# Optimization experiments

Measured on AMD Instinct MI355X. Metric: run time of the kernel, lower is better.

The kernel has to match this reference:

```python
import jax, jax.numpy as jnp
import numpy as np

NEG_INF = jnp.float32(-1e30)


def setup_inputs() -> dict:
    key = jax.random.key(0)
    ks = jax.random.split(key, 7)
    B, Lx, Lm, d = 4, 256, 256, 256
    return {
        "x": jax.random.normal(ks[0], (B, Lx, d), dtype=jnp.float32),
        "memory": jax.random.normal(ks[1], (B, Lm, d), dtype=jnp.float32),
        "memory_mask": jax.random.randint(ks[2], (B, Lm), 0, 2, dtype=jnp.int32),
        "ws1_w": jax.random.normal(ks[3], (d, d), dtype=jnp.float32) * 0.05,
        "ws1_b": jax.random.normal(ks[4], (d,), dtype=jnp.float32) * 0.05,
        "ws2_w": jax.random.normal(ks[5], (d, d), dtype=jnp.float32) * 0.05,
        "wst_w": jax.random.normal(ks[6], (1, d), dtype=jnp.float32) * 0.05,
    }


def reference(x, memory, memory_mask, ws1_w, ws1_b, ws2_w, wst_w):
    # x: [B, Lx, d], memory: [B, Lm, d]; torch Linear: y = x @ W.T + b
    item1 = jnp.einsum('bxd,ed->bxe', x, ws1_w) + ws1_b          # [B, Lx, d]
    item2 = jnp.einsum('bmd,ed->bme', memory, ws2_w)             # [B, Lm, d]
    item = jnp.tanh(item1[:, :, None, :] + item2[:, None, :, :])  # [B, Lx, Lm, d]
    S = jnp.einsum('bxmd,d->bxm', item, wst_w[0])                # [B, Lx, Lm]
    # agg_2_h uses the UNMASKED scores, softmax over Lx after transpose
    agg_2_h = jnp.einsum('bmx,bxd->bmd', jax.nn.softmax(S.transpose(0, 2, 1), axis=-1), x)
    # mask applied to S before the main attention readout
    S = jnp.where(memory_mask[:, None, :] == 0, NEG_INF, S)      # [B, Lx, Lm]
    out = jnp.einsum('bxm,bmd->bxd', jax.nn.softmax(S, axis=-1), memory)
    return (out, S, agg_2_h)
```

## Files before the change

kernel.cpp:

```cpp
#include <hip/hip_runtime.h>

static constexpr int NB = 4;
static constexpr int L  = 256;
static constexpr int D  = 256;

__device__ __forceinline__ float fast_rcp(float x) {
#if __has_builtin(__builtin_amdgcn_rcpf)
    return __builtin_amdgcn_rcpf(x);
#else
    return 1.0f / x;
#endif
}

__device__ __forceinline__ float fast_exp(float x) {
#if __has_builtin(__builtin_amdgcn_exp2f)
    return __builtin_amdgcn_exp2f(x * 1.4426950408889634f);
#else
    return __expf(x);
#endif
}

__device__ __forceinline__ float exp_2x(float x) {
#if __has_builtin(__builtin_amdgcn_exp2f)
    return __builtin_amdgcn_exp2f(x * 2.8853900817779268f);
#else
    return __expf(2.0f * x);
#endif
}

__global__ __launch_bounds__(256) void linear_kernel(
    const float* __restrict__ x, const float* __restrict__ mem,
    const float* __restrict__ w1, const float* __restrict__ b1,
    const float* __restrict__ w2,
    float* __restrict__ E1R, float* __restrict__ E2R)
{
    const int bid = blockIdx.x;
    const int rb  = (bid >> 3) * 32;
    const int cb  = (bid & 7) * 32;
    const int which = rb >= 1024;
    const int rloc  = which ? rb - 1024 : rb;
    const float* src = which ? mem : x;
    const float* W   = which ? w2  : w1;
    float*      dstR = which ? E2R : E1R;

    constexpr int P4 = 65;
    __shared__ __align__(16) float4 xs4[32 * P4];
    __shared__ __align__(16) float4 ws4[32 * P4];

    const int t = threadIdx.x;
    const float4* src4 = reinterpret_cast<const float4*>(src) + rloc * 64;
    const float4* Wg4  = reinterpret_cast<const float4*>(W)   + cb   * 64;
#pragma unroll
    for (int k = 0; k < 8; ++k) {
        int idx = k * 256 + t;
        int r = idx >> 6, c = idx & 63;
        xs4[r * P4 + c] = src4[r * 64 + c];
        ws4[r * P4 + c] = Wg4[r * 64 + c];
    }
    __syncthreads();

    const int rr = t >> 4, cc = t & 15;
    const float4* a0p = xs4 + rr * P4;
    const float4* a1p = xs4 + (rr + 16) * P4;
    const float4* w0p = ws4 + cc * P4;
    const float4* w1p = ws4 + (cc + 16) * P4;
    float acc00 = 0.f, acc01 = 0.f, acc10 = 0.f, acc11 = 0.f;
#pragma unroll 4
    for (int d4 = 0; d4 < 64; ++d4) {
        float4 a0 = a0p[d4], a1 = a1p[d4];
        float4 w0 = w0p[d4], w1 = w1p[d4];
        acc00 = fmaf(a0.x, w0.x, acc00); acc00 = fmaf(a0.y, w0.y, acc00);
        acc00 = fmaf(a0.z, w0.z, acc00); acc00 = fmaf(a0.w, w0.w, acc00);
        acc01 = fmaf(a0.x, w1.x, acc01); acc01 = fmaf(a0.y, w1.y, acc01);
        acc01 = fmaf(a0.z, w1.z, acc01); acc01 = fmaf(a0.w, w1.w, acc01);
        acc10 = fmaf(a1.x, w0.x, acc10); acc10 = fmaf(a1.y, w0.y, acc10);
        acc10 = fmaf(a1.z, w0.z, acc10); acc10 = fmaf(a1.w, w0.w, acc10);
        acc11 = fmaf(a1.x, w1.x, acc11); acc11 = fmaf(a1.y, w1.y, acc11);
        acc11 = fmaf(a1.z, w1.z, acc11); acc11 = fmaf(a1.w, w1.w, acc11);
    }
    const float bias0 = which ? 0.f : b1[cb + cc];
    const float bias1 = which ? 0.f : b1[cb + cc + 16];
    const int c0 = cb + cc, c1 = cb + cc + 16;
    const int rA = rloc + rr, rB = rloc + rr + 16;
    dstR[rA * D + c0] = exp_2x(acc00 + bias0);
    dstR[rA * D + c1] = exp_2x(acc01 + bias1);
    dstR[rB * D + c0] = exp_2x(acc10 + bias0);
    dstR[rB * D + c1] = exp_2x(acc11 + bias1);
}

__global__ __launch_bounds__(256) void score_kernel(
    const float* __restrict__ E1R, const float* __restrict__ E2R,
    const float* __restrict__ wst, const int* __restrict__ mask,
    float* __restrict__ Smask, float* __restrict__ ST)
{
    const int bid = blockIdx.x;
    const int p   = bid & 7, q = bid >> 3;
    const int b   = p >> 1;
    const int xg  = (q & 7) | ((p & 1) << 3);
    const int mg  = q >> 3;
    const int xt  = xg * 16, mt = mg * 32;
    const int base = b * L;
    const int t   = threadIdx.x;

    constexpr int P4 = 65;
    __shared__ __align__(16) float4 s1[16 * P4];
    __shared__ __align__(16) float4 s2[32 * P4];
    __shared__ float stile[32 * 17];

    const float4* e14 = reinterpret_cast<const float4*>(E1R) + (base + xt) * 64;
    const float4* e24 = reinterpret_cast<const float4*>(E2R) + (base + mt) * 64;
#pragma unroll
    for (int k = 0; k < 4; ++k) {
        int idx = k * 256 + t;
        int r = idx >> 6, c = idx & 63;
        s1[r * P4 + c] = e14[r * 64 + c];
    }
#pragma unroll
    for (int k = 0; k < 8; ++k) {
        int idx = k * 256 + t;
        int r = idx >> 6, c = idx & 63;
        s2[r * P4 + c] = e24[r * 64 + c];
    }
    __syncthreads();

    const float4* w4 = reinterpret_cast<const float4*>(wst);
    float W_tot;
    {
        float4 wv = w4[t & 63];
        float s = (wv.x + wv.y) + (wv.z + wv.w);
#pragma unroll
        for (int o = 32; o; o >>= 1) s += __shfl_xor(s, o);
        W_tot = s;
    }

    const int rr = t >> 4, cc = t & 15;
    const float4* ap  = s1 + rr * P4;
    const float4* b0p = s2 + cc * P4;
    const float4* b1p = s2 + (cc + 16) * P4;
    float acc0 = 0.f, acc1 = 0.f;
#pragma unroll 4
    for (int d4 = 0; d4 < 64; ++d4) {
        float4 a  = ap[d4];
        float4 b0 = b0p[d4], b1 = b1p[d4];
        float4 wv = w4[d4];
        acc0 = fmaf(wv.x, fast_rcp(fmaf(a.x, b0.x, 1.f)), acc0);
        acc0 = fmaf(wv.y, fast_rcp(fmaf(a.y, b0.y, 1.f)), acc0);
        acc0 = fmaf(wv.z, fast_rcp(fmaf(a.z, b0.z, 1.f)), acc0);
        acc0 = fmaf(wv.w, fast_rcp(fmaf(a.w, b0.w, 1.f)), acc0);
        acc1 = fmaf(wv.x, fast_rcp(fmaf(a.x, b1.x, 1.f)), acc1);
        acc1 = fmaf(wv.y, fast_rcp(fmaf(a.y, b1.y, 1.f)), acc1);
        acc1 = fmaf(wv.z, fast_rcp(fmaf(a.z, b1.z, 1.f)), acc1);
        acc1 = fmaf(wv.w, fast_rcp(fmaf(a.w, b1.w, 1.f)), acc1);
    }
    const float S0 = fmaf(-2.f, acc0, W_tot);
    const float S1 = fmaf(-2.f, acc1, W_tot);

    const int m0 = mt + cc, m1 = mt + cc + 16, x0 = xt + rr;
    Smask[((base + x0) << 8) + m0] = (mask[base + m0] == 0) ? -1e30f : S0;
    Smask[((base + x0) << 8) + m1] = (mask[base + m1] == 0) ? -1e30f : S1;

    stile[cc        * 17 + rr] = S0;
    stile[(cc + 16) * 17 + rr] = S1;
    __syncthreads();
#pragma unroll
    for (int k = 0; k < 2; ++k) {
        int idx = k * 256 + t;
        int mr = idx >> 4, xc = idx & 15;
        ST[((base + mt + mr) << 8) + xt + xc] = stile[mr * 17 + xc];
    }
}

__global__ __launch_bounds__(256) void attn_kernel(
    const float* __restrict__ x, const float* __restrict__ mem,
    const float* __restrict__ Smask, const float* __restrict__ ST,
    float* __restrict__ out, float* __restrict__ agg)
{
    const int bid  = blockIdx.x;
    const int p    = bid & 7, g = bid >> 3;
    const int side = p & 1,  b = p >> 1;
    const float* S = side ? ST : Smask;
    const float* V = side ? x  : mem;
    float*       o = side ? agg : out;
    const int base = b * L;
    const int row0 = g * 8;
    const int t = threadIdx.x, w = t >> 6, l = t & 63;

    __shared__ __align__(16) float  ps[8][L];
    __shared__ __align__(16) float4 part[8][4][64];

    float rs0, rs1;
#pragma unroll
    for (int rr = w, it = 0; rr < 8; rr += 4, ++it) {
        float4 sv = reinterpret_cast<const float4*>(S)[((base + row0 + rr) << 6) + l];
        float e0 = fast_exp(sv.x), e1 = fast_exp(sv.y);
        float e2 = fast_exp(sv.z), e3 = fast_exp(sv.w);
        reinterpret_cast<float4*>(ps[rr])[l] = make_float4(e0, e1, e2, e3);
        float s = (e0 + e1) + (e2 + e3);
#pragma unroll
        for (int off = 32; off; off >>= 1) s += __shfl_xor(s, off);
        if (it == 0) rs0 = fast_rcp(s); else rs1 = fast_rcp(s);
    }
    __syncthreads();

    const float4* V4 = reinterpret_cast<const float4*>(V) + base * 64;
    float4 acc[8];
#pragma unroll
    for (int r = 0; r < 8; ++r) acc[r] = make_float4(0.f, 0.f, 0.f, 0.f);

#pragma unroll 2
    for (int k4 = 0; k4 < 16; ++k4) {
        const int m0 = w * 64 + k4 * 4;
        float4 v0 = V4[(m0 + 0) * 64 + l];
        float4 v1 = V4[(m0 + 1) * 64 + l];
        float4 v2 = V4[(m0 + 2) * 64 + l];
        float4 v3 = V4[(m0 + 3) * 64 + l];
#pragma unroll
        for (int r = 0; r < 8; ++r) {
            float4 pr = *reinterpret_cast<const float4*>(&ps[r][m0]);
            acc[r].x = fmaf(pr.x, v0.x, acc[r].x); acc[r].y = fmaf(pr.x, v0.y, acc[r].y);
            acc[r].z = fmaf(pr.x, v0.z, acc[r].z); acc[r].w = fmaf(pr.x, v0.w, acc[r].w);
            acc[r].x = fmaf(pr.y, v1.x, acc[r].x); acc[r].y = fmaf(pr.y, v1.y, acc[r].y);
            acc[r].z = fmaf(pr.y, v1.z, acc[r].z); acc[r].w = fmaf(pr.y, v1.w, acc[r].w);
            acc[r].x = fmaf(pr.z, v2.x, acc[r].x); acc[r].y = fmaf(pr.z, v2.y, acc[r].y);
            acc[r].z = fmaf(pr.z, v2.z, acc[r].z); acc[r].w = fmaf(pr.z, v2.w, acc[r].w);
            acc[r].x = fmaf(pr.w, v3.x, acc[r].x); acc[r].y = fmaf(pr.w, v3.y, acc[r].y);
            acc[r].z = fmaf(pr.w, v3.z, acc[r].z); acc[r].w = fmaf(pr.w, v3.w, acc[r].w);
        }
    }
#pragma unroll
    for (int r = 0; r < 8; ++r) part[r][w][l] = acc[r];
    __syncthreads();

#pragma unroll
    for (int rr = w, it = 0; rr < 8; rr += 4, ++it) {
        float rs = (it == 0) ? rs0 : rs1;
        float4 q0 = part[rr][0][l], q1 = part[rr][1][l];
        float4 q2 = part[rr][2][l], q3 = part[rr][3][l];
        float4 ov;
        ov.x = ((q0.x + q1.x) + (q2.x + q3.x)) * rs;
        ov.y = ((q0.y + q1.y) + (q2.y + q3.y)) * rs;
        ov.z = ((q0.z + q1.z) + (q2.z + q3.z)) * rs;
        ov.w = ((q0.w + q1.w) + (q2.w + q3.w)) * rs;
        reinterpret_cast<float4*>(o)[((base + row0 + rr) << 6) + l] = ov;
    }
}

extern "C" void kernel_launch(void* const* d_in, const int* in_sizes, int n_in,
                              void* d_out, int out_size, void* d_ws, size_t ws_size,
                              hipStream_t stream)
{
    const float* x    = (const float*)d_in[0];
    const float* mem  = (const float*)d_in[1];
    const int*   mask = (const int*)  d_in[2];
    const float* w1   = (const float*)d_in[3];
    const float* b1   = (const float*)d_in[4];
    const float* w2   = (const float*)d_in[5];
    const float* wst  = (const float*)d_in[6];

    float* out   = (float*)d_out;
    float* Smask = out + NB * L * L;
    float* agg   = Smask + NB * L * L;

    float* E1R = (float*)d_ws;
    float* E2R = E1R + NB * L * D;
    float* ST  = E2R + NB * L * D;

    linear_kernel<<<512, 256, 0, stream>>>(x, mem, w1, b1, w2, E1R, E2R);
    score_kernel<<<512, 256, 0, stream>>>(E1R, E2R, wst, mask, Smask, ST);
    attn_kernel<<<256, 256, 0, stream>>>(x, mem, Smask, ST, out, agg);
}
```

Baseline: 35.39 us.

## Rewrite linear kernel without LDS tiling, using wave-uniform weight loads

The projection kernel drops its shared-memory staging. Each lane now computes one row, and each wave computes 4 output columns. The weight column index is forced wave-uniform via readfirstlane, so weight loads can become scalar loads while x rows are read straight from global memory. The aim is to remove the LDS fill, the barrier and LDS bandwidth pressure, at the cost of uncoalesced strided per-lane row reads from global/L2 and less data reuse per thread.

```diff
diff --git a/kernel.cpp b/kernel.cpp
--- a/kernel.cpp
+++ b/kernel.cpp
@@ -35,57 +35,52 @@
     float* __restrict__ E1R, float* __restrict__ E2R)
 {
     const int bid = blockIdx.x;
-    const int rb  = (bid >> 3) * 32;
-    const int cb  = (bid & 7) * 32;
-    const int which = rb >= 1024;
-    const int rloc  = which ? rb - 1024 : rb;
+    const int rg  = bid >> 4;
+    const int cg  = bid & 15;
+    const int rbase = rg * 64;
+    const int which = rbase >= 1024;
+    const int rloc  = which ? rbase - 1024 : rbase;
     const float* src = which ? mem : x;
     const float* W   = which ? w2  : w1;
-    float*      dstR = which ? E2R : E1R;
-
-    constexpr int P4 = 65;
-    __shared__ __align__(16) float4 xs4[32 * P4];
-    __shared__ __align__(16) float4 ws4[32 * P4];
-
-    const int t = threadIdx.x;
-    const float4* src4 = reinterpret_cast<const float4*>(src) + rloc * 64;
-    const float4* Wg4  = reinterpret_cast<const float4*>(W)   + cb   * 64;
-#pragma unroll
-    for (int k = 0; k < 8; ++k) {
-        int idx = k * 256 + t;
-        int r = idx >> 6, c = idx & 63;
-        xs4[r * P4 + c] = src4[r * 64 + c];
-        ws4[r * P4 + c] = Wg4[r * 64 + c];
-    }
-    __syncthreads();
-
-    const int rr = t >> 4, cc = t & 15;
-    const float4* a0p = xs4 + rr * P4;
-    const float4* a1p = xs4 + (rr + 16) * P4;
-    const float4* w0p = ws4 + cc * P4;
-    const float4* w1p = ws4 + (cc + 16) * P4;
-    float acc00 = 0.f, acc01 = 0.f, acc10 = 0.f, acc11 = 0.f;
+    float*       dst = which ? E2R : E1R;
+
+    const int t    = threadIdx.x;
+    const int wv   = t >> 6;
+    const int lane = t & 63;
+    const int row  = rloc + lane;
+
+    const int c0u = __builtin_amdgcn_readfirstlane(cg * 16 + wv * 4);
+
+    const float4* x4 = reinterpret_cast<const float4*>(src) + row * 64;
+    const float4* Wp = reinterpret_cast<const float4*>(W) + c0u * 64;
+
+    float acc0 = 0.f, acc1 = 0.f, acc2 = 0.f, acc3 = 0.f;
 #pragma unroll 4
     for (int d4 = 0; d4 < 64; ++d4) {
-        float4 a0 = a0p[d4], a1 = a1p[d4];
-        float4 w0 = w0p[d4], w1 = w1p[d4];
-        acc00 = fmaf(a0.x, w0.x, acc00); acc00 = fmaf(a0.y, w0.y, acc00);
-        acc00 = fmaf(a0.z, w0.z, acc00); acc00 = fmaf(a0.w, w0.w, acc00);
-        acc01 = fmaf(a0.x, w1.x, acc01); acc01 = fmaf(a0.y, w1.y, acc01);
-        acc01 = fmaf(a0.z, w1.z, acc01); acc01 = fmaf(a0.w, w1.w, acc01);
-        acc10 = fmaf(a1.x, w0.x, acc10); acc10 = fmaf(a1.y, w0.y, acc10);
-        acc10 = fmaf(a1.z, w0.z, acc10); acc10 = fmaf(a1.w, w0.w, acc10);
-        acc11 = fmaf(a1.x, w1.x, acc11); acc11 = fmaf(a1.y, w1.y, acc11);
-        acc11 = fmaf(a1.z, w1.z, acc11); acc11 = fmaf(a1.w, w1.w, acc11);
-    }
-    const float bias0 = which ? 0.f : b1[cb + cc];
-    const float bias1 = which ? 0.f : b1[cb + cc + 16];
-    const int c0 = cb + cc, c1 = cb + cc + 16;
-    const int rA = rloc + rr, rB = rloc + rr + 16;
-    dstR[rA * D + c0] = exp_2x(acc00 + bias0);
-    dstR[rA * D + c1] = exp_2x(acc01 + bias1);
-    dstR[rB * D + c0] = exp_2x(acc10 + bias0);
-    dstR[rB * D + c1] = exp_2x(acc11 + bias1);
+        float4 xv = x4[d4];
+        float4 wA = Wp[d4];
+        float4 wB = Wp[64  + d4];
+        float4 wC = Wp[128 + d4];
+        float4 wD = Wp[192 + d4];
+        acc0 = fmaf(xv.x, wA.x, acc0); acc0 = fmaf(xv.y, wA.y, acc0);
+        acc0 = fmaf(xv.z, wA.z, acc0); acc0 = fmaf(xv.w, wA.w, acc0);
+        acc1 = fmaf(xv.x, wB.x, acc1); acc1 = fmaf(xv.y, wB.y, acc1);
+        acc1 = fmaf(xv.z, wB.z, acc1); acc1 = fmaf(xv.w, wB.w, acc1);
+        acc2 = fmaf(xv.x, wC.x, acc2); acc2 = fmaf(xv.y, wC.y, acc2);
+        acc2 = fmaf(xv.z, wC.z, acc2); acc2 = fmaf(xv.w, wC.w, acc2);
+        acc3 = fmaf(xv.x, wD.x, acc3); acc3 = fmaf(xv.y, wD.y, acc3);
+        acc3 = fmaf(xv.z, wD.z, acc3); acc3 = fmaf(xv.w, wD.w, acc3);
+    }
+    float bias0 = 0.f, bias1 = 0.f, bias2 = 0.f, bias3 = 0.f;
+    if (!which) {
+        bias0 = b1[c0u];     bias1 = b1[c0u + 1];
+        bias2 = b1[c0u + 2]; bias3 = b1[c0u + 3];
+    }
+    float* drow = dst + row * D + c0u;
+    drow[0] = exp_2x(acc0 + bias0);
+    drow[1] = exp_2x(acc1 + bias1);
+    drow[2] = exp_2x(acc2 + bias2);
+    drow[3] = exp_2x(acc3 + bias3);
 }
 
 __global__ __launch_bounds__(256) void score_kernel(
```

After: 43.75 us. 23.6% more time.
